# Optimization experiments

Measured on AMD Instinct MI355X. Metric: run time of the kernel, lower is better.

## Reference

```python
import jax, jax.numpy as jnp
import numpy as np
import math

D_MODEL = 1024
HEAD_DIM = 256
GAMMA = 0.9


def setup_inputs() -> dict:
    key = jax.random.key(0)
    k1, k2, k3, k4 = jax.random.split(key, 4)
    B, L = 4, 4096
    x = jax.random.normal(k1, (B, L, D_MODEL), dtype=jnp.float32)
    s = 1.0 / math.sqrt(D_MODEL)
    W_Q = jax.random.normal(k2, (HEAD_DIM, D_MODEL), dtype=jnp.float32) * s
    W_K = jax.random.normal(k3, (HEAD_DIM, D_MODEL), dtype=jnp.float32) * s
    W_V = jax.random.normal(k4, (HEAD_DIM, D_MODEL), dtype=jnp.float32) * s
    return {"x": x, "W_Q": W_Q, "W_K": W_K, "W_V": W_V}


def _decay_mask(L: int, gamma: float) -> jnp.ndarray:
    # D[i,j] = gamma^(i-j) if i >= j else 0
    idx = jnp.arange(L)
    diff = idx[:, None] - idx[None, :]
    return jnp.where(diff >= 0, jnp.power(jnp.float32(gamma), diff.astype(jnp.float32)), 0.0)


def reference(x, W_Q, W_K, W_V):
    B, L, _ = x.shape
    Q = jnp.einsum('bld,hd->blh', x, W_Q)  # (B,L,H)
    K = jnp.einsum('bld,hd->blh', x, W_K)
    V = jnp.einsum('bld,hd->blh', x, W_V)
    D = _decay_mask(L, GAMMA)  # (L,L)
    scores = jnp.einsum('bih,bjh->bij', Q, K) * D[None, :, :]
    scores = scores / jnp.sqrt(jnp.float32(HEAD_DIM))
    return jnp.einsum('bij,bjh->bih', scores, V)  # (B,L,H)
```

## Files before the change

### kernel.cpp

```cpp
#include <hip/hip_runtime.h>

typedef unsigned short u16;
typedef __attribute__((ext_vector_type(8))) short bf16x8;
typedef __attribute__((ext_vector_type(4))) float f32x4;
typedef __attribute__((ext_vector_type(4))) unsigned short u16x4;

#define DEVI __device__ __forceinline__

constexpr float L2GAMMA = -0.15200309344504997f;
constexpr float INV_SQRT_H = 0.0625f;

DEVI u16 f2bf(float x) {
  union { float f; unsigned u; } v; v.f = x;
  unsigned r = v.u + 0x7FFFu + ((v.u >> 16) & 1u);
  return (u16)(r >> 16);
}

__global__ void cvt_x_kernel(const float4* __restrict__ src, u16x4* __restrict__ dst, int n4) {
  int stride = gridDim.x * blockDim.x;
  for (int i = blockIdx.x * blockDim.x + threadIdx.x; i < n4; i += stride) {
    float4 v = src[i];
    u16x4 o; o.x = f2bf(v.x); o.y = f2bf(v.y); o.z = f2bf(v.z); o.w = f2bf(v.w);
    dst[i] = o;
  }
}

__global__ void cvt_w_kernel(const float4* __restrict__ wq, const float4* __restrict__ wk,
                             const float4* __restrict__ wv, u16x4* __restrict__ dst) {
  int i = blockIdx.x * blockDim.x + threadIdx.x;
  int w = i >> 16, off = i & 65535;
  const float4* s = (w == 0) ? wq : ((w == 1) ? wk : wv);
  float4 v = s[off];
  u16x4 o; o.x = f2bf(v.x); o.y = f2bf(v.y); o.z = f2bf(v.z); o.w = f2bf(v.w);
  dst[(w << 16) + off] = o;
}

__global__ __launch_bounds__(256) void qkv_gemm_kernel(const u16* __restrict__ Xb, const u16* __restrict__ Wb,
                                                       u16* __restrict__ Qb, u16* __restrict__ Kb,
                                                       u16* __restrict__ Vt) {
  __shared__ u16 Alds[128 * 64];
  __shared__ u16 Blds[128 * 64];
  const int linear = blockIdx.x + blockIdx.y * 6;
  const int rl = (linear & 7) * 96 + (linear >> 3);
  const int nt = rl % 6;
  const int m0 = (rl / 6) * 128;
  const int n0 = nt * 128;
  const int tid = threadIdx.x;
  const int wid = tid >> 6, lane = tid & 63;
  const int wm = wid >> 1, wn = wid & 1;
  const int lrow = lane & 15, lkg = lane >> 4;
  const int srow = lane >> 3;
  const int scol = ((lane & 7) ^ srow) << 3;

  f32x4 acc[4][4] = {};

  for (int kt = 0; kt < 16; ++kt) {
    const int k0 = kt * 64;
#pragma unroll
    for (int r = 0; r < 4; ++r) {
      const int chunk = wid * 4 + r;
      const int row = chunk * 8 + srow;
      const u16* gA = Xb + (size_t)(m0 + row) * 1024 + k0 + scol;
      const u16* gB = Wb + (size_t)(n0 + row) * 1024 + k0 + scol;
      __builtin_amdgcn_global_load_lds((const __attribute__((address_space(1))) void*)gA,
                                       (__attribute__((address_space(3))) void*)&Alds[chunk * 512], 16, 0, 0);
      __builtin_amdgcn_global_load_lds((const __attribute__((address_space(1))) void*)gB,
                                       (__attribute__((address_space(3))) void*)&Blds[chunk * 512], 16, 0, 0);
    }
    __syncthreads();
#pragma unroll
    for (int kk = 0; kk < 2; ++kk) {
      bf16x8 a[4], b[4];
      const int sw = ((kk * 4 + lkg) ^ (lrow & 7)) << 3;
#pragma unroll
      for (int mf = 0; mf < 4; ++mf) a[mf] = *(const bf16x8*)&Alds[(wm * 64 + mf * 16 + lrow) * 64 + sw];
#pragma unroll
      for (int nf = 0; nf < 4; ++nf) b[nf] = *(const bf16x8*)&Blds[(wn * 64 + nf * 16 + lrow) * 64 + sw];
#pragma unroll
      for (int mf = 0; mf < 4; ++mf)
#pragma unroll
        for (int nf = 0; nf < 4; ++nf)
          acc[mf][nf] = __builtin_amdgcn_mfma_f32_16x16x32_bf16(a[mf], b[nf], acc[mf][nf], 0, 0, 0);
    }
    __syncthreads();
  }

  const int rbase = lkg * 4;
  if (nt < 4) {
    u16* Dst = (nt < 2) ? Qb : Kb;
    const int cb = (nt < 2) ? n0 : (n0 - 256);
#pragma unroll
    for (int mf = 0; mf < 4; ++mf)
#pragma unroll
      for (int nf = 0; nf < 4; ++nf) {
        const int gm = m0 + wm * 64 + mf * 16 + rbase;
        const int c = cb + wn * 64 + nf * 16 + lrow;
#pragma unroll
        for (int r = 0; r < 4; ++r) Dst[(size_t)(gm + r) * 256 + c] = f2bf(acc[mf][nf][r]);
      }
  } else {
#pragma unroll
    for (int mf = 0; mf < 4; ++mf)
#pragma unroll
      for (int nf = 0; nf < 4; ++nf) {
        const int gm = m0 + wm * 64 + mf * 16 + rbase;
        const int h = n0 - 512 + wn * 64 + nf * 16 + lrow;
        const int bb = gm >> 12, l = gm & 4095;
        u16x4 pk;
        pk.x = f2bf(acc[mf][nf][0]); pk.y = f2bf(acc[mf][nf][1]);
        pk.z = f2bf(acc[mf][nf][2]); pk.w = f2bf(acc[mf][nf][3]);
        *(u16x4*)&Vt[((size_t)bb * 256 + h) * 4096 + l] = pk;
      }
  }
}

__global__ __launch_bounds__(256) void attn_kernel(const u16* __restrict__ Qb, const u16* __restrict__ Kb,
                                                   const u16* __restrict__ Vt, float* __restrict__ out) {
  __shared__ u16 Plds[32 * 72];
  const int raw = blockIdx.x;
  const int aid = (raw & 7) * 64 + (raw >> 3);
  const int b = aid >> 7;
  const int qt = aid & 127;
  const int qb = qt * 32;
  const int tid = threadIdx.x;
  const int wid = tid >> 6, lane = tid & 63;
  const int lrow = lane & 15, lkg = lane >> 4, lk = lkg * 8;
  const size_t bQK = (size_t)b * 4096 * 256;

  bf16x8 qf[2][8];
#pragma unroll
  for (int mf = 0; mf < 2; ++mf) {
    const u16* Qrow = Qb + bQK + (size_t)(qb + mf * 16 + lrow) * 256;
#pragma unroll
    for (int kf = 0; kf < 8; ++kf) qf[mf][kf] = *(const bf16x8*)&Qrow[kf * 32 + lk];
  }

  int kstart = qb - 256; if (kstart < 0) kstart = 0; kstart &= ~63;
  const int njt = (qb + 32 - kstart + 63) >> 6;

  f32x4 oacc[2][4] = {};

  for (int jt = 0; jt < njt; ++jt) {
    const int kb = kstart + jt * 64;
    f32x4 s[2] = {};
    const u16* Krow = Kb + bQK + (size_t)(kb + wid * 16 + lrow) * 256;
#pragma unroll
    for (int kf = 0; kf < 8; ++kf) {
      const bf16x8 kfr = *(const bf16x8*)&Krow[kf * 32 + lk];
      s[0] = __builtin_amdgcn_mfma_f32_16x16x32_bf16(qf[0][kf], kfr, s[0], 0, 0, 0);
      s[1] = __builtin_amdgcn_mfma_f32_16x16x32_bf16(qf[1][kf], kfr, s[1], 0, 0, 0);
    }
    const int kg = kb + wid * 16 + lrow;
#pragma unroll
    for (int mf = 0; mf < 2; ++mf) {
      const int qg = qb + mf * 16 + lkg * 4;
#pragma unroll
      for (int r = 0; r < 4; ++r) {
        const int d = qg + r - kg;
        const float pv = (d >= 0) ? s[mf][r] * exp2f((float)d * L2GAMMA) * INV_SQRT_H : 0.0f;
        Plds[(mf * 16 + lkg * 4 + r) * 72 + wid * 16 + lrow] = f2bf(pv);
      }
    }
    __syncthreads();
#pragma unroll
    for (int ks = 0; ks < 2; ++ks) {
      bf16x8 pa[2];
      pa[0] = *(const bf16x8*)&Plds[(lrow) * 72 + ks * 32 + lk];
      pa[1] = *(const bf16x8*)&Plds[(16 + lrow) * 72 + ks * 32 + lk];
#pragma unroll
      for (int nf = 0; nf < 4; ++nf) {
        const bf16x8 vb = *(const bf16x8*)&Vt[((size_t)b * 256 + wid * 64 + nf * 16 + lrow) * 4096 + kb + ks * 32 + lk];
        oacc[0][nf] = __builtin_amdgcn_mfma_f32_16x16x32_bf16(pa[0], vb, oacc[0][nf], 0, 0, 0);
        oacc[1][nf] = __builtin_amdgcn_mfma_f32_16x16x32_bf16(pa[1], vb, oacc[1][nf], 0, 0, 0);
      }
    }
    __syncthreads();
  }

#pragma unroll
  for (int mf = 0; mf < 2; ++mf) {
    float* obase = out + ((size_t)b * 4096 + qb + mf * 16 + lkg * 4) * 256 + wid * 64 + lrow;
#pragma unroll
    for (int nf = 0; nf < 4; ++nf)
#pragma unroll
      for (int r = 0; r < 4; ++r)
        obase[(size_t)r * 256 + nf * 16] = oacc[mf][nf][r];
  }
}

extern "C" void kernel_launch(void* const* d_in, const int* in_sizes, int n_in,
                              void* d_out, int out_size, void* d_ws, size_t ws_size,
                              hipStream_t stream) {
  const float* x  = (const float*)d_in[0];
  const float* wq = (const float*)d_in[1];
  const float* wk = (const float*)d_in[2];
  const float* wv = (const float*)d_in[3];
  float* out = (float*)d_out;
  char* ws = (char*)d_ws;
  u16* Xb = (u16*)(ws);
  u16* Wb = (u16*)(ws + (size_t)33554432);
  u16* Qb = (u16*)(ws + (size_t)35127296);
  u16* Kb = (u16*)(ws + (size_t)43515904);
  u16* Vt = (u16*)(ws + (size_t)51904512);

  hipLaunchKernelGGL(cvt_x_kernel, dim3(2048), dim3(256), 0, stream,
                     (const float4*)x, (u16x4*)Xb, 4194304);
  hipLaunchKernelGGL(cvt_w_kernel, dim3(768), dim3(256), 0, stream,
                     (const float4*)wq, (const float4*)wk, (const float4*)wv, (u16x4*)Wb);
  hipLaunchKernelGGL(qkv_gemm_kernel, dim3(6, 128), dim3(256), 0, stream, Xb, Wb, Qb, Kb, Vt);
  hipLaunchKernelGGL(attn_kernel, dim3(512), dim3(256), 0, stream, Qb, Kb, Vt, out);
}
```

Measured before the change: 92.43 us.

## Fuse x fp32-to-bf16 conversion into QKV GEMM with double-buffered LDS

```diff
diff --git a/kernel.cpp b/kernel.cpp
--- a/kernel.cpp
+++ b/kernel.cpp
@@ -1,6 +1,7 @@
 #include <hip/hip_runtime.h>
 
 typedef unsigned short u16;
+typedef unsigned int u32;
 typedef __attribute__((ext_vector_type(8))) short bf16x8;
 typedef __attribute__((ext_vector_type(4))) float f32x4;
 typedef __attribute__((ext_vector_type(4))) unsigned short u16x4;
@@ -16,13 +17,10 @@
   return (u16)(r >> 16);
 }
 
-__global__ void cvt_x_kernel(const float4* __restrict__ src, u16x4* __restrict__ dst, int n4) {
-  int stride = gridDim.x * blockDim.x;
-  for (int i = blockIdx.x * blockDim.x + threadIdx.x; i < n4; i += stride) {
-    float4 v = src[i];
-    u16x4 o; o.x = f2bf(v.x); o.y = f2bf(v.y); o.z = f2bf(v.z); o.w = f2bf(v.w);
-    dst[i] = o;
-  }
+DEVI u32 pack2bf(float f0, float f1) {
+  u32 u0 = __float_as_uint(f0) + 0x8000u;
+  u32 u1 = __float_as_uint(f1) + 0x8000u;
+  return __builtin_amdgcn_perm(u1, u0, 0x07060302u);
 }
 
 __global__ void cvt_w_kernel(const float4* __restrict__ wq, const float4* __restrict__ wk,
@@ -35,11 +33,11 @@
   dst[(w << 16) + off] = o;
 }
 
-__global__ __launch_bounds__(256) void qkv_gemm_kernel(const u16* __restrict__ Xb, const u16* __restrict__ Wb,
-                                                       u16* __restrict__ Qb, u16* __restrict__ Kb,
-                                                       u16* __restrict__ Vt) {
-  __shared__ u16 Alds[128 * 64];
-  __shared__ u16 Blds[128 * 64];
+__global__ __launch_bounds__(256, 2) void qkv_gemm_kernel(const float* __restrict__ Xf, const u16* __restrict__ Wb,
+                                                          u16* __restrict__ Qb, u16* __restrict__ Kb,
+                                                          u16* __restrict__ Vt) {
+  __shared__ u16 Alds[2][128 * 64];
+  __shared__ u16 Blds[2][128 * 64];
   const int linear = blockIdx.x + blockIdx.y * 6;
   const int rl = (linear & 7) * 96 + (linear >> 3);
   const int nt = rl % 6;
@@ -49,40 +47,73 @@
   const int wid = tid >> 6, lane = tid & 63;
   const int wm = wid >> 1, wn = wid & 1;
   const int lrow = lane & 15, lkg = lane >> 4;
-  const int srow = lane >> 3;
-  const int scol = ((lane & 7) ^ srow) << 3;
+  const int l8 = lane >> 3, l7 = lane & 7;
+  const int scol = (l7 ^ l8) << 3;
+  const int acu = ((l7 << 3) ^ (l8 << 3));
+
+  const float* agbase = Xf + (size_t)(m0 + wid * 32 + l8) * 1024 + l7 * 8;
+  float4 areg[8];
+
+#define LOADA(KT) do { const float* g_ = agbase + (KT) * 64; \
+  _Pragma("unroll") for (int p_ = 0; p_ < 4; ++p_) { \
+    areg[2*p_]   = *(const float4*)(g_ + (size_t)p_ * 8 * 1024); \
+    areg[2*p_+1] = *(const float4*)(g_ + (size_t)p_ * 8 * 1024 + 4); } } while (0)
+
+#define STAGEB(KT, BUF) do { const int k0_ = (KT) * 64; \
+  _Pragma("unroll") for (int r_ = 0; r_ < 4; ++r_) { \
+    const int chunk_ = wid * 4 + r_; \
+    const u16* gB_ = Wb + (size_t)(n0 + chunk_ * 8 + l8) * 1024 + k0_ + scol; \
+    __builtin_amdgcn_global_load_lds((const __attribute__((address_space(1))) void*)gB_, \
+        (__attribute__((address_space(3))) void*)&Blds[BUF][chunk_ * 512], 16, 0, 0); } } while (0)
+
+#define CVTWRITE(BUF) do { \
+  _Pragma("unroll") for (int p_ = 0; p_ < 4; ++p_) { \
+    const int r_ = wid * 32 + p_ * 8 + l8; \
+    u32 w0 = pack2bf(areg[2*p_].x, areg[2*p_].y); \
+    u32 w1 = pack2bf(areg[2*p_].z, areg[2*p_].w); \
+    u32 w2 = pack2bf(areg[2*p_+1].x, areg[2*p_+1].y); \
+    u32 w3 = pack2bf(areg[2*p_+1].z, areg[2*p_+1].w); \
+    uint4 pk_; pk_.x = w0; pk_.y = w1; pk_.z = w2; pk_.w = w3; \
+    *(uint4*)&Alds[BUF][r_ * 64 + acu] = pk_; } } while (0)
 
   f32x4 acc[4][4] = {};
 
+  LOADA(0);
+  STAGEB(0, 0);
+  CVTWRITE(0);
+  asm volatile("s_waitcnt vmcnt(0) lgkmcnt(0)" ::: "memory");
+  __builtin_amdgcn_s_barrier();
+
+  int cur = 0;
   for (int kt = 0; kt < 16; ++kt) {
-    const int k0 = kt * 64;
-#pragma unroll
-    for (int r = 0; r < 4; ++r) {
-      const int chunk = wid * 4 + r;
-      const int row = chunk * 8 + srow;
-      const u16* gA = Xb + (size_t)(m0 + row) * 1024 + k0 + scol;
-      const u16* gB = Wb + (size_t)(n0 + row) * 1024 + k0 + scol;
-      __builtin_amdgcn_global_load_lds((const __attribute__((address_space(1))) void*)gA,
-                                       (__attribute__((address_space(3))) void*)&Alds[chunk * 512], 16, 0, 0);
-      __builtin_amdgcn_global_load_lds((const __attribute__((address_space(1))) void*)gB,
-                                       (__attribute__((address_space(3))) void*)&Blds[chunk * 512], 16, 0, 0);
-    }
-    __syncthreads();
-#pragma unroll
-    for (int kk = 0; kk < 2; ++kk) {
-      bf16x8 a[4], b[4];
-      const int sw = ((kk * 4 + lkg) ^ (lrow & 7)) << 3;
-#pragma unroll
-      for (int mf = 0; mf < 4; ++mf) a[mf] = *(const bf16x8*)&Alds[(wm * 64 + mf * 16 + lrow) * 64 + sw];
-#pragma unroll
-      for (int nf = 0; nf < 4; ++nf) b[nf] = *(const bf16x8*)&Blds[(wn * 64 + nf * 16 + lrow) * 64 + sw];
-#pragma unroll
-      for (int mf = 0; mf < 4; ++mf)
-#pragma unroll
-        for (int nf = 0; nf < 4; ++nf)
-          acc[mf][nf] = __builtin_amdgcn_mfma_f32_16x16x32_bf16(a[mf], b[nf], acc[mf][nf], 0, 0, 0);
-    }
-    __syncthreads();
+    const int nxt = cur ^ 1;
+    if (kt < 15) { LOADA(kt + 1); STAGEB(kt + 1, nxt); }
+    __builtin_amdgcn_sched_barrier(0);
+    {
+      const u16* Ab = Alds[cur];
+      const u16* Bb = Blds[cur];
+#pragma unroll
+      for (int kk = 0; kk < 2; ++kk) {
+        bf16x8 a[4], b[4];
+        const int sw = ((kk * 4 + lkg) ^ (lrow & 7)) << 3;
+#pragma unroll
+        for (int mf = 0; mf < 4; ++mf) a[mf] = *(const bf16x8*)&Ab[(wm * 64 + mf * 16 + lrow) * 64 + sw];
+#pragma unroll
+        for (int nf = 0; nf < 4; ++nf) b[nf] = *(const bf16x8*)&Bb[(wn * 64 + nf * 16 + lrow) * 64 + sw];
+#pragma unroll
+        for (int mf = 0; mf < 4; ++mf)
+#pragma unroll
+          for (int nf = 0; nf < 4; ++nf)
+            acc[mf][nf] = __builtin_amdgcn_mfma_f32_16x16x32_bf16(a[mf], b[nf], acc[mf][nf], 0, 0, 0);
+      }
+    }
+    __builtin_amdgcn_sched_barrier(0);
+    if (kt < 15) {
+      CVTWRITE(nxt);
+      asm volatile("s_waitcnt vmcnt(0) lgkmcnt(0)" ::: "memory");
+      __builtin_amdgcn_s_barrier();
+    }
+    cur = nxt;
   }
 
   const int rbase = lkg * 4;
@@ -197,16 +228,13 @@
   const float* wv = (const float*)d_in[3];
   float* out = (float*)d_out;
   char* ws = (char*)d_ws;
-  u16* Xb = (u16*)(ws);
-  u16* Wb = (u16*)(ws + (size_t)33554432);
-  u16* Qb = (u16*)(ws + (size_t)35127296);
-  u16* Kb = (u16*)(ws + (size_t)43515904);
-  u16* Vt = (u16*)(ws + (size_t)51904512);
-
-  hipLaunchKernelGGL(cvt_x_kernel, dim3(2048), dim3(256), 0, stream,
-                     (const float4*)x, (u16x4*)Xb, 4194304);
+  u16* Wb = (u16*)(ws);
+  u16* Qb = (u16*)(ws + (size_t)1572864);
+  u16* Kb = (u16*)(ws + (size_t)9961472);
+  u16* Vt = (u16*)(ws + (size_t)18350080);
+
   hipLaunchKernelGGL(cvt_w_kernel, dim3(768), dim3(256), 0, stream,
                      (const float4*)wq, (const float4*)wk, (const float4*)wv, (u16x4*)Wb);
-  hipLaunchKernelGGL(qkv_gemm_kernel, dim3(6, 128), dim3(256), 0, stream, Xb, Wb, Qb, Kb, Vt);
+  hipLaunchKernelGGL(qkv_gemm_kernel, dim3(6, 128), dim3(256), 0, stream, x, Wb, Qb, Kb, Vt);
   hipLaunchKernelGGL(attn_kernel, dim3(512), dim3(256), 0, stream, Qb, Kb, Vt, out);
 }
```

Measured after the change: 88.46 us. -4.3%, faster.

## Fuse x fp32-to-bf16 conversion into QKV GEMM via fp32 LDS staging

Applied to the files above, without the earlier changes.

```diff
diff --git a/kernel.cpp b/kernel.cpp
--- a/kernel.cpp
+++ b/kernel.cpp
@@ -1,11 +1,14 @@
 #include <hip/hip_runtime.h>
 
 typedef unsigned short u16;
+typedef unsigned int u32;
 typedef __attribute__((ext_vector_type(8))) short bf16x8;
 typedef __attribute__((ext_vector_type(4))) float f32x4;
 typedef __attribute__((ext_vector_type(4))) unsigned short u16x4;
 
 #define DEVI __device__ __forceinline__
+#define AS1 __attribute__((address_space(1)))
+#define AS3 __attribute__((address_space(3)))
 
 constexpr float L2GAMMA = -0.15200309344504997f;
 constexpr float INV_SQRT_H = 0.0625f;
@@ -16,13 +19,10 @@
   return (u16)(r >> 16);
 }
 
-__global__ void cvt_x_kernel(const float4* __restrict__ src, u16x4* __restrict__ dst, int n4) {
-  int stride = gridDim.x * blockDim.x;
-  for (int i = blockIdx.x * blockDim.x + threadIdx.x; i < n4; i += stride) {
-    float4 v = src[i];
-    u16x4 o; o.x = f2bf(v.x); o.y = f2bf(v.y); o.z = f2bf(v.z); o.w = f2bf(v.w);
-    dst[i] = o;
-  }
+DEVI u32 pack2bf(float f0, float f1) {
+  u32 u0 = __float_as_uint(f0) + 0x8000u;
+  u32 u1 = __float_as_uint(f1) + 0x8000u;
+  return __builtin_amdgcn_perm(u1, u0, 0x07060302u);
 }
 
 __global__ void cvt_w_kernel(const float4* __restrict__ wq, const float4* __restrict__ wk,
@@ -35,13 +35,13 @@
   dst[(w << 16) + off] = o;
 }
 
-__global__ __launch_bounds__(256) void qkv_gemm_kernel(const u16* __restrict__ Xb, const u16* __restrict__ Wb,
-                                                       u16* __restrict__ Qb, u16* __restrict__ Kb,
-                                                       u16* __restrict__ Vt) {
-  __shared__ u16 Alds[128 * 64];
-  __shared__ u16 Blds[128 * 64];
-  const int linear = blockIdx.x + blockIdx.y * 6;
-  const int rl = (linear & 7) * 96 + (linear >> 3);
+__global__ __launch_bounds__(256, 3) void qkv_gemm_kernel(const float* __restrict__ Xf, const u16* __restrict__ Wb,
+                                                          u16* __restrict__ Qb, u16* __restrict__ Kb,
+                                                          u16* __restrict__ Vt) {
+  __shared__ float Af[128 * 32];
+  __shared__ u16 Bl[128 * 32];
+  const int lin = blockIdx.x;
+  const int rl = (lin & 7) * 96 + (lin >> 3);
   const int nt = rl % 6;
   const int m0 = (rl / 6) * 128;
   const int n0 = nt * 128;
@@ -49,39 +49,51 @@
   const int wid = tid >> 6, lane = tid & 63;
   const int wm = wid >> 1, wn = wid & 1;
   const int lrow = lane & 15, lkg = lane >> 4;
-  const int srow = lane >> 3;
-  const int scol = ((lane & 7) ^ srow) << 3;
+  const int arow_in = lane >> 3;
+  const int aslot_src = (lane & 7) ^ arow_in;
+  const int brow_in = lane >> 2;
+  const int bslot_src = (lane & 3) ^ ((lane >> 3) & 3);
 
   f32x4 acc[4][4] = {};
 
-  for (int kt = 0; kt < 16; ++kt) {
-    const int k0 = kt * 64;
+  for (int kt = 0; kt < 32; ++kt) {
+    const int k0 = kt * 32;
 #pragma unroll
     for (int r = 0; r < 4; ++r) {
-      const int chunk = wid * 4 + r;
-      const int row = chunk * 8 + srow;
-      const u16* gA = Xb + (size_t)(m0 + row) * 1024 + k0 + scol;
-      const u16* gB = Wb + (size_t)(n0 + row) * 1024 + k0 + scol;
-      __builtin_amdgcn_global_load_lds((const __attribute__((address_space(1))) void*)gA,
-                                       (__attribute__((address_space(3))) void*)&Alds[chunk * 512], 16, 0, 0);
-      __builtin_amdgcn_global_load_lds((const __attribute__((address_space(1))) void*)gB,
-                                       (__attribute__((address_space(3))) void*)&Blds[chunk * 512], 16, 0, 0);
-    }
-    __syncthreads();
-#pragma unroll
-    for (int kk = 0; kk < 2; ++kk) {
-      bf16x8 a[4], b[4];
-      const int sw = ((kk * 4 + lkg) ^ (lrow & 7)) << 3;
-#pragma unroll
-      for (int mf = 0; mf < 4; ++mf) a[mf] = *(const bf16x8*)&Alds[(wm * 64 + mf * 16 + lrow) * 64 + sw];
-#pragma unroll
-      for (int nf = 0; nf < 4; ++nf) b[nf] = *(const bf16x8*)&Blds[(wn * 64 + nf * 16 + lrow) * 64 + sw];
-#pragma unroll
-      for (int mf = 0; mf < 4; ++mf)
-#pragma unroll
-        for (int nf = 0; nf < 4; ++nf)
-          acc[mf][nf] = __builtin_amdgcn_mfma_f32_16x16x32_bf16(a[mf], b[nf], acc[mf][nf], 0, 0, 0);
-    }
+      const int c = wid * 4 + r;
+      const float* g = Xf + (size_t)(m0 + c * 8 + arow_in) * 1024 + k0 + aslot_src * 4;
+      __builtin_amdgcn_global_load_lds((const AS1 void*)g, (AS3 void*)&Af[c * 256], 16, 0, 0);
+    }
+#pragma unroll
+    for (int r = 0; r < 2; ++r) {
+      const int c = wid * 2 + r;
+      const u16* g = Wb + (size_t)(n0 + c * 16 + brow_in) * 1024 + k0 + bslot_src * 8;
+      __builtin_amdgcn_global_load_lds((const AS1 void*)g, (AS3 void*)&Bl[c * 512], 16, 0, 0);
+    }
+    __syncthreads();
+    bf16x8 a[4], b[4];
+#pragma unroll
+    for (int mf = 0; mf < 4; ++mf) {
+      const int row = wm * 64 + mf * 16 + lrow;
+      const int e0 = (2 * lkg) ^ (lrow & 7);
+      const float4 lo = *(const float4*)&Af[row * 32 + e0 * 4];
+      const float4 hi = *(const float4*)&Af[row * 32 + (e0 ^ 1) * 4];
+      union { u32 w[4]; bf16x8 v; } ua;
+      ua.w[0] = pack2bf(lo.x, lo.y); ua.w[1] = pack2bf(lo.z, lo.w);
+      ua.w[2] = pack2bf(hi.x, hi.y); ua.w[3] = pack2bf(hi.z, hi.w);
+      a[mf] = ua.v;
+    }
+#pragma unroll
+    for (int nf = 0; nf < 4; ++nf) {
+      const int row = wn * 64 + nf * 16 + lrow;
+      const int s = lkg ^ ((row >> 1) & 3);
+      b[nf] = *(const bf16x8*)&Bl[row * 32 + s * 8];
+    }
+#pragma unroll
+    for (int mf = 0; mf < 4; ++mf)
+#pragma unroll
+      for (int nf = 0; nf < 4; ++nf)
+        acc[mf][nf] = __builtin_amdgcn_mfma_f32_16x16x32_bf16(a[mf], b[nf], acc[mf][nf], 0, 0, 0);
     __syncthreads();
   }
 
@@ -197,16 +209,13 @@
   const float* wv = (const float*)d_in[3];
   float* out = (float*)d_out;
   char* ws = (char*)d_ws;
-  u16* Xb = (u16*)(ws);
-  u16* Wb = (u16*)(ws + (size_t)33554432);
-  u16* Qb = (u16*)(ws + (size_t)35127296);
-  u16* Kb = (u16*)(ws + (size_t)43515904);
-  u16* Vt = (u16*)(ws + (size_t)51904512);
-
-  hipLaunchKernelGGL(cvt_x_kernel, dim3(2048), dim3(256), 0, stream,
-                     (const float4*)x, (u16x4*)Xb, 4194304);
+  u16* Wb = (u16*)(ws);
+  u16* Qb = (u16*)(ws + (size_t)1572864);
+  u16* Kb = (u16*)(ws + (size_t)9961472);
+  u16* Vt = (u16*)(ws + (size_t)18350080);
+
   hipLaunchKernelGGL(cvt_w_kernel, dim3(768), dim3(256), 0, stream,
                      (const float4*)wq, (const float4*)wk, (const float4*)wv, (u16x4*)Wb);
-  hipLaunchKernelGGL(qkv_gemm_kernel, dim3(6, 128), dim3(256), 0, stream, Xb, Wb, Qb, Kb, Vt);
+  hipLaunchKernelGGL(qkv_gemm_kernel, dim3(768), dim3(256), 0, stream, x, Wb, Qb, Kb, Vt);
   hipLaunchKernelGGL(attn_kernel, dim3(512), dim3(256), 0, stream, Qb, Kb, Vt, out);
 }
```

Measured after the change: 76.61 us. 1.21x faster.
